# Optimization experiments

Hardware: AMD Instinct MI355X
Metric: run time of the kernel (lower is better)

## Reference

```python
import jax, jax.numpy as jnp
import numpy as np

B, T, D_IN, H, D = 4, 4096, 1024, 16, 64


def setup_inputs() -> dict:
    key = jax.random.key(0)
    k1, k2, k3 = jax.random.split(key, 3)
    inputs = jax.random.normal(k1, (B, T, D_IN), dtype=jnp.float32)
    kv_kernel = jax.random.normal(k2, (D_IN, H, D, 2), dtype=jnp.float32) * (1.0 / np.sqrt(D_IN))
    q_kernel = jax.random.normal(k3, (H, D), dtype=jnp.float32) * (1.0 / np.sqrt(D))
    return {"inputs": inputs, "kv_kernel": kv_kernel, "q_kernel": q_kernel}


def _associate(a, b):
    # Online-softmax combine on packed tuples [m(1), u(1), w(D)] along last axis.
    ma, ua, wa = a[..., :1], a[..., 1:2], a[..., 2:]
    mb, ub, wb = b[..., :1], b[..., 1:2], b[..., 2:]
    m = jnp.maximum(ma, mb)
    ea = jnp.exp(ma - m)
    eb = jnp.exp(mb - m)
    u = ua * ea + ub * eb
    w = wa * ea + wb * eb
    return jnp.concatenate([m, u, w], axis=-1)


def reference(inputs, kv_kernel, q_kernel):
    # inputs: (B,T,D_in); kv_kernel: (D_in,H,D,2); q_kernel: (H,D)
    kv = jnp.einsum('bti,ihdk->bthdk', inputs, kv_kernel)
    kv = jax.nn.relu(kv)  # activation; dropout disabled (inference)
    k = kv[..., 0]  # (B,T,H,D)
    v = kv[..., 1]  # (B,T,H,D)
    st = jnp.einsum('hd,bthd->bth', q_kernel, k)[..., None]  # (B,T,H,1)
    u_init = jnp.ones_like(st)  # exp(s - m) with m = s
    elems = jnp.concatenate([st, u_init, v], axis=-1)  # (B,T,H,D+2)
    o = jax.lax.associative_scan(_associate, elems, axis=1)
    c = o[..., 1:2]  # running denominator
    a = o[..., 2:]   # running numerator (B,T,H,D)
    h = a / c
    # concat_heads=False -> sum over heads
    return jnp.sum(h, axis=-2)  # (B,T,D)
```

## Files before the change

### kernel.cpp

```cpp
#include <hip/hip_runtime.h>
#include <hip/hip_bf16.h>
#include <math.h>

#define B_   4
#define T_   4096
#define DIN_ 1024
#define H_   16
#define D_   64
#define M_   (B_*T_)
#define N_   (H_*D_*2)
#define K_   DIN_
#define C_   64
#define CL_  (T_/C_)

typedef unsigned short u16;
typedef __attribute__((ext_vector_type(8))) short short8_t;
typedef __attribute__((ext_vector_type(4))) float float4_t;

__device__ __forceinline__ u16 f2bf(float f) {
  unsigned int x = __float_as_uint(f);
  x += 0x7fffu + ((x >> 16) & 1u);
  return (u16)(x >> 16);
}
__device__ __forceinline__ float bf2f(unsigned int u) {
  return __uint_as_float((u & 0xffffu) << 16);
}
__device__ __forceinline__ unsigned pk_bf16(float x, float y) {
  float2 f; f.x = x; f.y = y;
  union { __hip_bfloat162 h2; unsigned u; } c;
  c.h2 = __float22bfloat162_rn(f);
  return c.u;
}

__device__ __forceinline__ void g2l16(const u16* g, u16* l) {
  __builtin_amdgcn_global_load_lds(
      (const __attribute__((address_space(1))) void*)g,
      (__attribute__((address_space(3))) void*)l, 16, 0, 0);
}

__global__ __launch_bounds__(256)
void prep(const float* __restrict__ inputs, const float* __restrict__ kvk,
          u16* __restrict__ aB, u16* __restrict__ wBt) {
  __shared__ float tile[32][33];
  int bid = blockIdx.x;
  int tid = threadIdx.x;
  if (bid < 8192) {
    int i = bid * 256 + tid;
    const float4* src = (const float4*)inputs;
    float4 a = src[2*i], b = src[2*i+1];
    uint4 o;
    o.x = pk_bf16(a.x, a.y);
    o.y = pk_bf16(a.z, a.w);
    o.z = pk_bf16(b.x, b.y);
    o.w = pk_bf16(b.z, b.w);
    ((uint4*)aB)[i] = o;
  } else {
    int b2 = bid - 8192;
    int kb = (b2 & 31) * 32;
    int nb = (b2 >> 5) * 32;
    int r  = tid >> 3;
    int c4 = (tid & 7) * 4;
    float4 v = *(const float4*)&kvk[(size_t)(kb + r) * N_ + nb + c4];
    tile[r][c4+0] = v.x; tile[r][c4+1] = v.y; tile[r][c4+2] = v.z; tile[r][c4+3] = v.w;
    __syncthreads();
    uint2 o;
    o.x = pk_bf16(tile[c4+0][r], tile[c4+1][r]);
    o.y = pk_bf16(tile[c4+2][r], tile[c4+3][r]);
    *(uint2*)&wBt[(size_t)(nb + r) * K_ + kb + c4] = o;
  }
}


#define FENCE asm volatile("" ::: "memory")
#define KBAR do { FENCE; __builtin_amdgcn_s_barrier(); FENCE; } while (0)

#define STAGE_A(P, KT, CC) do { \
  g2l16(gA + ((size_t)((CC)*64      ) * K_ + (KT)*64), lds + (P)*16384 +        (CC)*4096 + wv*512); \
  g2l16(gA + ((size_t)((CC)*64 + 128) * K_ + (KT)*64), lds + (P)*16384 + 8192 + (CC)*4096 + wv*512); \
} while (0)

#define STAGE_B(P, KT, HH) do { \
  g2l16(gB + ((size_t)((HH)*128     ) * K_ + (KT)*64), lds + 32768 + (P)*16384 + (HH)*8192 +        wv*512); \
  g2l16(gB + ((size_t)((HH)*128 + 64) * K_ + (KT)*64), lds + 32768 + (P)*16384 + (HH)*8192 + 4096 + wv*512); \
} while (0)

#define READ_A(P, MH) do { _Pragma("unroll") \
  for (int il_ = 0; il_ < 4; ++il_) { \
    const int o_ = (P)*16384 + aBase + (MH)*4096 + il_*1024; \
    af[il_][0] = *(const short8_t*)&lds[o_ + s0]; \
    af[il_][1] = *(const short8_t*)&lds[o_ + s1]; \
  } } while (0)

#define READ_B(P, NH) do { _Pragma("unroll") \
  for (int jl_ = 0; jl_ < 2; ++jl_) { \
    const int o_ = (P)*16384 + (NH)*8192 + bBase + jl_*1024; \
    bfr[NH][jl_][0] = *(const short8_t*)&lds[o_ + s0]; \
    bfr[NH][jl_][1] = *(const short8_t*)&lds[o_ + s1]; \
  } } while (0)

#define MFMA_Q(MH, NH) do { \
  __builtin_amdgcn_s_setprio(1); \
  _Pragma("unroll") for (int kk_ = 0; kk_ < 2; ++kk_) \
  _Pragma("unroll") for (int il_ = 0; il_ < 4; ++il_) \
  _Pragma("unroll") for (int jl_ = 0; jl_ < 2; ++jl_) \
    acc[(MH)*4+il_][(NH)*2+jl_] = __builtin_amdgcn_mfma_f32_16x16x32_bf16( \
        af[il_][kk_], bfr[NH][jl_][kk_], acc[(MH)*4+il_][(NH)*2+jl_], 0, 0, 0); \
  __builtin_amdgcn_s_setprio(0); \
} while (0)

__global__ __launch_bounds__(512, 2)
void gemm_kv(const u16* __restrict__ A, const u16* __restrict__ Bt,
             const float* __restrict__ q,
             float* __restrict__ pbuf, u16* __restrict__ vbuf,
             float* __restrict__ aggU, float* __restrict__ aggW) {
  extern __shared__ __align__(16) char smem[];
  u16* lds = (u16*)smem;

  const int tid  = threadIdx.x;
  const int wv   = tid >> 6;
  const int lane = tid & 63;
  const int quad = lane >> 4;
  const int l16  = lane & 15;
  const int wr   = wv >> 2;
  const int wc   = wv & 3;

  const int g  = blockIdx.x;
  const int wg = (g & 7) * 64 + (g >> 3);
  const int nt = wg & 7;
  const int mt = wg >> 3;
  const int bm = mt * 256;
  const int bn = nt * 256;

  const int tr   = tid >> 3;
  const int gran = tid & 7;
  const u16* gA = A  + (size_t)(bm + tr) * K_ + ((gran ^ (tr & 7)) * 8);
  const u16* gB = Bt + (size_t)(bn + tr) * K_ + ((gran ^ (tr & 7)) * 8);

  const int s0 = ((quad    ) ^ (l16 & 7)) * 8;
  const int s1 = ((quad + 4) ^ (l16 & 7)) * 8;
  const int aBase = wr * 8192 + l16 * 64;
  const int bBase = 32768 + wc * 2048 + l16 * 64;

  float4_t acc[8][4] = {};
  short8_t af[4][2];
  short8_t bfr[2][2][2];

  STAGE_A(0, 0, 0); STAGE_A(0, 0, 1);
  STAGE_B(0, 0, 0); STAGE_B(0, 0, 1);
  STAGE_A(1, 1, 0); STAGE_B(1, 1, 0);
  asm volatile("s_waitcnt vmcnt(4)" ::: "memory");
  KBAR;

#pragma unroll 1
  for (int it = 0; it < 8; ++it) {
    const int kt1 = 2*it + 1, kt2 = 2*it + 2, kt3 = 2*it + 3;
    const bool more = (it < 7);
    READ_A(0, 0); READ_B(0, 0);
    STAGE_A(1, kt1, 1);
    KBAR;
    MFMA_Q(0, 0);
    KBAR;
    READ_B(0, 1);
    STAGE_B(1, kt1, 1);
    KBAR;
    MFMA_Q(0, 1);
    KBAR;
    READ_A(0, 1);
    if (more) STAGE_A(0, kt2, 0);
    KBAR;
    MFMA_Q(1, 0);
    KBAR;
    if (more) STAGE_B(0, kt2, 0);
    KBAR;
    MFMA_Q(1, 1);
    if (more) asm volatile("s_waitcnt vmcnt(4)" ::: "memory");
    else      asm volatile("s_waitcnt vmcnt(0)" ::: "memory");
    KBAR;
    READ_A(1, 0); READ_B(1, 0);
    if (more) STAGE_A(0, kt2, 1);
    KBAR;
    MFMA_Q(0, 0);
    KBAR;
    READ_B(1, 1);
    if (more) STAGE_B(0, kt2, 1);
    KBAR;
    MFMA_Q(0, 1);
    KBAR;
    READ_A(1, 1);
    if (more) STAGE_A(1, kt3, 0);
    KBAR;
    MFMA_Q(1, 0);
    KBAR;
    if (more) STAGE_B(1, kt3, 0);
    KBAR;
    MFMA_Q(1, 1);
    if (more) asm volatile("s_waitcnt vmcnt(4)" ::: "memory");
    KBAR;
  }

  u16*   vtile = (u16*)smem;
  float* sred  = (float*)(smem + 73728);
  float* pS    = (float*)(smem + 108544);

  float qv[2][2];
#pragma unroll
  for (int nh = 0; nh < 2; ++nh)
#pragma unroll
    for (int jl = 0; jl < 2; ++jl)
      qv[nh][jl] = q[nt*128 + nh*64 + wc*16 + jl*8 + (l16 >> 1)];

#pragma unroll
  for (int nh = 0; nh < 2; ++nh) {
#pragma unroll
    for (int i = 0; i < 8; ++i) {
#pragma unroll
      for (int r = 0; r < 4; ++r) {
        const int t = wr*128 + i*16 + quad*4 + r;
        const float x0 = fmaxf(acc[i][nh*2+0][r], 0.f);
        const float x1 = fmaxf(acc[i][nh*2+1][r], 0.f);
        if (l16 & 1) {
          const int d0 = (wc*32 + l16) >> 1;
          vtile[(nh*256 + t)*72 + d0    ] = f2bf(x0);
          vtile[(nh*256 + t)*72 + d0 + 8] = f2bf(x1);
        }
        float ps = qv[nh][0]*x0 + qv[nh][1]*x1;
        ps += __shfl_xor(ps, 2);
        if ((l16 & 3) == 0)
          sred[(nh*256 + t)*17 + wc*4 + (l16 >> 2)] = ps;
      }
    }
  }
  __syncthreads();

  const int b  = mt >> 4;
  const int t0 = (mt & 15) * 256;
  {
    const int hh = tid >> 8;
    const int t  = tid & 255;
    float s = 0.f;
#pragma unroll
    for (int k = 0; k < 16; ++k) s += sred[(hh*256 + t)*17 + k];
    float p = __expf(fminf(fmaxf(s, -60.f), 60.f));
    pS[hh*256 + t] = p;
    pbuf[(size_t)(b*H_ + nt*2 + hh) * T_ + t0 + t] = p;
  }
  __syncthreads();

  {
    const int hh = wv >> 2;
    const int ch = wv & 3;
    float U = 0.f, W = 0.f;
#pragma unroll 8
    for (int i2 = 0; i2 < CL_; ++i2) {
      const int t = ch*CL_ + i2;
      float p = pS[hh*256 + t];
      float v = bf2f(vtile[(hh*256 + t)*72 + lane]);
      U += p;
      W += p * v;
    }
    const int bh  = b*H_ + nt*2 + hh;
    const int blk = bh*C_ + (mt & 15)*4 + ch;
    aggW[(size_t)blk * D_ + lane] = W;
    if (lane == 0) aggU[blk] = U;
  }
  {
    const int rr = tid >> 3;
    const int d0 = (tid & 7) * 8;
#pragma unroll
    for (int k2 = 0; k2 < 8; ++k2) {
      const int row = rr + 64*k2;
      const int hh  = row >> 8;
      const int t   = row & 255;
      uint4 val = *(const uint4*)&vtile[(hh*256 + t)*72 + d0];
      *(uint4*)&vbuf[((size_t)(b*H_ + nt*2 + hh) * T_ + t0 + t) * D_ + d0] = val;
    }
  }
}

__global__ __launch_bounds__(1024)
void scan_pass3(const u16* __restrict__ vbuf, const float* __restrict__ pbuf,
                const float* __restrict__ aggU, const float* __restrict__ aggW,
                float* __restrict__ out) {
  __shared__ float pS[H_][CL_];
  __shared__ float wbuf[H_][8][D_ + 1];
  int bc = blockIdx.x;
  int b  = bc >> 6;
  int c  = bc & (C_ - 1);
  int tid  = threadIdx.x;
  int h    = tid >> 6;
  int lane = tid & 63;
  int bh   = b * H_ + h;
  int t0   = c * CL_;

  pS[h][lane] = pbuf[(size_t)bh * T_ + t0 + lane];

  float U = 0.f, W = 0.f;
  for (int j = 0; j < c; ++j) {
    int idx = bh * C_ + j;
    U += aggU[idx];
    W += aggW[(size_t)idx * D_ + lane];
  }
  __syncthreads();

  const u16* vp = vbuf + ((size_t)bh * T_ + t0) * D_ + lane;
  for (int gg = 0; gg < 8; ++gg) {
#pragma unroll
    for (int ii = 0; ii < 8; ++ii) {
      int i = gg * 8 + ii;
      float p = pS[h][i];
      float v = bf2f(vp[i * D_]);
      U += p;
      W += p * v;
      wbuf[h][ii][lane] = __fdividef(W, U);
    }
    __syncthreads();
    if (tid < 512) {
      int ii = tid >> 6, dd = tid & 63;
      float acc = 0.f;
#pragma unroll
      for (int hh = 0; hh < H_; ++hh) acc += wbuf[hh][ii][dd];
      out[((size_t)b * T_ + t0 + gg*8 + ii) * D_ + dd] = acc;
    }
    __syncthreads();
  }
}

extern "C" void kernel_launch(void* const* d_in, const int* in_sizes, int n_in,
                              void* d_out, int out_size, void* d_ws, size_t ws_size,
                              hipStream_t stream) {
  const float* inputs = (const float*)d_in[0];
  const float* kvk    = (const float*)d_in[1];
  const float* qk     = (const float*)d_in[2];
  float* out = (float*)d_out;
  char* ws = (char*)d_ws;

  u16*   aB   = (u16*)ws;
  u16*   wBt  = (u16*)(ws + 33554432);
  u16*   vb   = (u16*)(ws + 37748736);
  float* pb   = (float*)(ws + 71303168);
  float* aggU = (float*)(ws + 72351744);
  float* aggW = (float*)(ws + 72368128);

  prep<<<10240, 256, 0, stream>>>(inputs, kvk, aB, wBt);
  gemm_kv<<<512, 512, 131072, stream>>>(aB, wBt, qk, pb, vb, aggU, aggW);
  scan_pass3<<<B_*C_, 1024, 0, stream>>>(vb, pb, aggU, aggW, out);
}
```

Measured before the change: 204.1 us.

## Store V transposed and swizzled in LDS and global, prefetch V in scan

The V tile in shared memory becomes d-major with an XOR swizzle on the time index, written as packed bf16 pairs. vbuf in global memory becomes a layout of 8-timestep groups per d, so the scan kernel can load all 64 timesteps per lane as eight 16-byte vector loads up front instead of 64 scalar 2-byte loads. The per-chunk U aggregate now comes from a warp reduction over p rather than from the W loop. This changes the layout contract between the two kernels and the LDS offsets, and adds bank-conflict and layout-correctness risk.

New measurement: 205.0 us. No clear change (+0.4%).

```diff
diff --git a/kernel.cpp b/kernel.cpp
--- a/kernel.cpp
+++ b/kernel.cpp
@@ -108,6 +108,8 @@
   __builtin_amdgcn_s_setprio(0); \
 } while (0)
 
+#define VST_ 264
+
 __global__ __launch_bounds__(512, 2)
 void gemm_kv(const u16* __restrict__ A, const u16* __restrict__ Bt,
              const float* __restrict__ q,
@@ -199,8 +201,8 @@
   }
 
   u16*   vtile = (u16*)smem;
-  float* sred  = (float*)(smem + 73728);
-  float* pS    = (float*)(smem + 108544);
+  float* sred  = (float*)(smem + 67584);
+  float* pS    = (float*)(smem + 102400);
 
   float qv[2][2];
 #pragma unroll
@@ -213,20 +215,32 @@
   for (int nh = 0; nh < 2; ++nh) {
 #pragma unroll
     for (int i = 0; i < 8; ++i) {
+      float x0[4], x1[4];
 #pragma unroll
       for (int r = 0; r < 4; ++r) {
-        const int t = wr*128 + i*16 + quad*4 + r;
-        const float x0 = fmaxf(acc[i][nh*2+0][r], 0.f);
-        const float x1 = fmaxf(acc[i][nh*2+1][r], 0.f);
-        if (l16 & 1) {
-          const int d0 = (wc*32 + l16) >> 1;
-          vtile[(nh*256 + t)*72 + d0    ] = f2bf(x0);
-          vtile[(nh*256 + t)*72 + d0 + 8] = f2bf(x1);
+        x0[r] = fmaxf(acc[i][nh*2+0][r], 0.f);
+        x1[r] = fmaxf(acc[i][nh*2+1][r], 0.f);
+      }
+      const int tb = wr*128 + i*16 + quad*4;
+      if (l16 & 1) {
+        const int d0 = wc*16 + (l16 >> 1);
+        const int sA = ((d0 >> 3) & 3) << 3;
+        const int sB = (((d0+8) >> 3) & 3) << 3;
+#pragma unroll
+        for (int rp = 0; rp < 4; rp += 2) {
+          const int t = tb + rp;
+          *(unsigned*)&vtile[(nh*64 + d0    )*VST_ + (t ^ sA)] = pk_bf16(x0[rp], x0[rp+1]);
+          *(unsigned*)&vtile[(nh*64 + d0 + 8)*VST_ + (t ^ sB)] = pk_bf16(x1[rp], x1[rp+1]);
         }
-        float ps = qv[nh][0]*x0 + qv[nh][1]*x1;
-        ps += __shfl_xor(ps, 2);
-        if ((l16 & 3) == 0)
-          sred[(nh*256 + t)*17 + wc*4 + (l16 >> 2)] = ps;
+      } else {
+#pragma unroll
+        for (int r = 0; r < 4; ++r) {
+          const int t = tb + r;
+          float ps = qv[nh][0]*x0[r] + qv[nh][1]*x1[r];
+          ps += __shfl_xor(ps, 2);
+          if ((l16 & 3) == 0)
+            sred[(nh*256 + t)*17 + wc*4 + (l16 >> 2)] = ps;
+        }
       }
     }
   }
@@ -243,36 +257,47 @@
     float p = __expf(fminf(fmaxf(s, -60.f), 60.f));
     pS[hh*256 + t] = p;
     pbuf[(size_t)(b*H_ + nt*2 + hh) * T_ + t0 + t] = p;
+    float u = p;
+#pragma unroll
+    for (int off = 32; off; off >>= 1) u += __shfl_down(u, off);
+    if (lane == 0) {
+      const int ch = (tid >> 6) & 3;
+      aggU[(b*H_ + nt*2 + hh)*C_ + (mt & 15)*4 + ch] = u;
+    }
   }
   __syncthreads();
 
   {
     const int hh = wv >> 2;
     const int ch = wv & 3;
-    float U = 0.f, W = 0.f;
+    const int d  = lane;
+    const int sK = ((d >> 3) & 3) << 3;
+    float W = 0.f;
 #pragma unroll 8
     for (int i2 = 0; i2 < CL_; ++i2) {
       const int t = ch*CL_ + i2;
       float p = pS[hh*256 + t];
-      float v = bf2f(vtile[(hh*256 + t)*72 + lane]);
-      U += p;
+      float v = bf2f(vtile[(hh*64 + d)*VST_ + (t ^ sK)]);
       W += p * v;
     }
-    const int bh  = b*H_ + nt*2 + hh;
-    const int blk = bh*C_ + (mt & 15)*4 + ch;
-    aggW[(size_t)blk * D_ + lane] = W;
-    if (lane == 0) aggU[blk] = U;
+    const int blk = (b*H_ + nt*2 + hh)*C_ + (mt & 15)*4 + ch;
+    aggW[(size_t)blk * D_ + d] = W;
   }
   {
-    const int rr = tid >> 3;
-    const int d0 = (tid & 7) * 8;
-#pragma unroll
-    for (int k2 = 0; k2 < 8; ++k2) {
-      const int row = rr + 64*k2;
-      const int hh  = row >> 8;
-      const int t   = row & 255;
-      uint4 val = *(const uint4*)&vtile[(hh*256 + t)*72 + d0];
-      *(uint4*)&vbuf[((size_t)(b*H_ + nt*2 + hh) * T_ + t0 + t) * D_ + d0] = val;
+    const int d  = tid & 63;
+    const int kk = tid >> 6;
+    const int sK = ((d >> 3) & 3) << 3;
+    const int tc0 = (mt & 15) * 32;
+#pragma unroll
+    for (int hh = 0; hh < 2; ++hh) {
+#pragma unroll
+      for (int j = 0; j < 4; ++j) {
+        const int k  = kk + 8*j;
+        const int gI = (k*8) ^ sK;
+        uint4 val = *(const uint4*)&vtile[(hh*64 + d)*VST_ + gI];
+        const size_t bh = (size_t)(b*H_ + nt*2 + hh);
+        *(uint4*)&vbuf[((bh*512 + tc0 + k)*64 + d)*8] = val;
+      }
     }
   }
 }
@@ -294,6 +319,13 @@
 
   pS[h][lane] = pbuf[(size_t)bh * T_ + t0 + lane];
 
+  uint4 vq[8];
+  {
+    const uint4* vb4 = (const uint4*)vbuf + ((size_t)bh*512 + (t0 >> 3))*64 + lane;
+#pragma unroll
+    for (int gq = 0; gq < 8; ++gq) vq[gq] = vb4[(size_t)gq * 64];
+  }
+
   float U = 0.f, W = 0.f;
   for (int j = 0; j < c; ++j) {
     int idx = bh * C_ + j;
@@ -302,13 +334,13 @@
   }
   __syncthreads();
 
-  const u16* vp = vbuf + ((size_t)bh * T_ + t0) * D_ + lane;
   for (int gg = 0; gg < 8; ++gg) {
+    unsigned wa[4] = { vq[gg].x, vq[gg].y, vq[gg].z, vq[gg].w };
 #pragma unroll
     for (int ii = 0; ii < 8; ++ii) {
-      int i = gg * 8 + ii;
-      float p = pS[h][i];
-      float v = bf2f(vp[i * D_]);
+      float p = pS[h][gg*8 + ii];
+      unsigned word = wa[ii >> 1];
+      float v = bf2f((ii & 1) ? (word >> 16) : word);
       U += p;
       W += p * v;
       wbuf[h][ii][lane] = __fdividef(W, U);
```
